# Kernel optimization log

Hardware: AMD Instinct MI355X
Metric: run time of the kernel (lower is better)

## Reference

```python
import jax, jax.numpy as jnp
import numpy as np

NUM_HEADS = 8
OUT_FEATS = 128
D_HEAD = OUT_FEATS // NUM_HEADS
N_NODES = 50000
N_EDGES = 600000
IN_FEATS = 128


def setup_inputs() -> dict:
    key = jax.random.key(0)
    ks = jax.random.split(key, 10)
    h = jax.random.normal(ks[0], (N_NODES, IN_FEATS), dtype=jnp.float32)
    src = jax.random.randint(ks[1], (N_EDGES,), 0, N_NODES)
    dst = jax.random.randint(ks[2], (N_EDGES,), 0, N_NODES)
    s = 1.0 / np.sqrt(IN_FEATS)
    W_Q = jax.random.normal(ks[3], (IN_FEATS, OUT_FEATS), dtype=jnp.float32) * s
    W_K = jax.random.normal(ks[4], (IN_FEATS, OUT_FEATS), dtype=jnp.float32) * s
    W_V = jax.random.normal(ks[5], (IN_FEATS, OUT_FEATS), dtype=jnp.float32) * s
    b_Q = jnp.zeros((OUT_FEATS,), dtype=jnp.float32)
    b_K = jnp.zeros((OUT_FEATS,), dtype=jnp.float32)
    b_V = jnp.zeros((OUT_FEATS,), dtype=jnp.float32)
    return {"h": h, "W_Q": W_Q, "b_Q": b_Q, "W_K": W_K, "b_K": b_K,
            "W_V": W_V, "b_V": b_V, "src": src, "dst": dst}


def _graph_conv(h, W, b, src, dst, norm_src, norm_dst):
    # DGL GraphConv, norm='both': D_dst^{-1/2} * A * D_src^{-1/2} * (h W) + b
    x = (h * norm_src[:, None]) @ W                              # [N, F]
    agg = jax.ops.segment_sum(x[src], dst, num_segments=h.shape[0])
    return agg * norm_dst[:, None] + b


def reference(h, W_Q, b_Q, W_K, b_K, W_V, b_V, src, dst):
    N = h.shape[0]
    ones = jnp.ones(src.shape[0], dtype=h.dtype)
    deg_out = jax.ops.segment_sum(ones, src, num_segments=N)   # out-degree (src side)
    deg_in = jax.ops.segment_sum(ones, dst, num_segments=N)    # in-degree (dst side)
    norm_src = jax.lax.rsqrt(jnp.clip(deg_out, 1.0))
    norm_dst = jax.lax.rsqrt(jnp.clip(deg_in, 1.0))

    Q = jax.nn.relu(_graph_conv(h, W_Q, b_Q, src, dst, norm_src, norm_dst))
    K = jax.nn.relu(_graph_conv(h, W_K, b_K, src, dst, norm_src, norm_dst))
    V = jax.nn.relu(_graph_conv(h, W_V, b_V, src, dst, norm_src, norm_dst))

    Qh = Q.reshape(N, NUM_HEADS, D_HEAD)
    Kh = K.reshape(N, NUM_HEADS, D_HEAD)
    Vh = V.reshape(N, NUM_HEADS, D_HEAD)

    # edge-wise scores: K at src dotted with Q at dst, per head
    score = jnp.sum(Kh[src] * Qh[dst], axis=-1, keepdims=True)   # [E, H, 1]
    score = jnp.exp(jnp.clip(score / np.sqrt(D_HEAD), -10.0, 10.0))

    wV = jax.ops.segment_sum(Vh[src] * score, dst, num_segments=N)  # [N, H, Dh]
    z = jax.ops.segment_sum(score, dst, num_segments=N)             # [N, H, 1]
    return wV / (z + 1e-6)
```

## Files before the change

kernel.cpp:

```cpp
#include <hip/hip_runtime.h>

#define INF  128
#define OUTF 128
#define NH   8
#define DHD  16
#define CAP  48

typedef __attribute__((ext_vector_type(8))) short bf16x8;
typedef __attribute__((ext_vector_type(4))) float f32x4;

__device__ __forceinline__ float bf16_to_f32(unsigned short u) {
    union { unsigned int i; float f; } v;
    v.i = ((unsigned int)u) << 16;
    return v.f;
}
__device__ __forceinline__ unsigned short f32_to_bf16(float f) {
    union { float f; unsigned int i; } v;
    v.f = f;
    unsigned int x = v.i;
    return (unsigned short)((x + 0x7fffu + ((x >> 16) & 1u)) >> 16);
}

__global__ void k_front(const int* __restrict__ src, const int* __restrict__ dst,
                        int* __restrict__ deg_out, int* __restrict__ cursor,
                        int* __restrict__ edge_src, int E, int SB, int HB,
                        const float* __restrict__ h, unsigned short* __restrict__ h_b, int N,
                        const float* __restrict__ Wq, const float* __restrict__ Wk,
                        const float* __restrict__ Wv, unsigned short* __restrict__ frag) {
    if (blockIdx.x < (unsigned)SB) {
        int t = blockIdx.x * 256 + threadIdx.x;
        int e0 = t * 4;
        if (e0 + 4 <= E) {
            int4 s4 = *reinterpret_cast<const int4*>(src + e0);
            int4 d4 = *reinterpret_cast<const int4*>(dst + e0);
            atomicAdd(&deg_out[s4.x], 1);
            atomicAdd(&deg_out[s4.y], 1);
            atomicAdd(&deg_out[s4.z], 1);
            atomicAdd(&deg_out[s4.w], 1);
            int p0 = atomicAdd(&cursor[d4.x], 1);
            int p1 = atomicAdd(&cursor[d4.y], 1);
            int p2 = atomicAdd(&cursor[d4.z], 1);
            int p3 = atomicAdd(&cursor[d4.w], 1);
            if (p0 < CAP) edge_src[d4.x * CAP + p0] = s4.x;
            if (p1 < CAP) edge_src[d4.y * CAP + p1] = s4.y;
            if (p2 < CAP) edge_src[d4.z * CAP + p2] = s4.z;
            if (p3 < CAP) edge_src[d4.w * CAP + p3] = s4.w;
        } else {
            for (int e = e0; e < E; ++e) {
                int s = src[e];
                int d = dst[e];
                atomicAdd(&deg_out[s], 1);
                int p = atomicAdd(&cursor[d], 1);
                if (p < CAP) edge_src[d * CAP + p] = s;
            }
        }
    } else if (blockIdx.x < (unsigned)(SB + HB)) {
        int t = (blockIdx.x - SB) * 256 + threadIdx.x;
        if (t < N * (INF / 8)) {
            const float4* p = reinterpret_cast<const float4*>(h + (size_t)t * 8);
            float4 v0 = p[0], v1 = p[1];
            uint4 o;
            o.x = (unsigned int)f32_to_bf16(v0.x) | ((unsigned int)f32_to_bf16(v0.y) << 16);
            o.y = (unsigned int)f32_to_bf16(v0.z) | ((unsigned int)f32_to_bf16(v0.w) << 16);
            o.z = (unsigned int)f32_to_bf16(v1.x) | ((unsigned int)f32_to_bf16(v1.y) << 16);
            o.w = (unsigned int)f32_to_bf16(v1.z) | ((unsigned int)f32_to_bf16(v1.w) << 16);
            *reinterpret_cast<uint4*>(h_b + (size_t)t * 8) = o;
        }
    } else {
        int t = (blockIdx.x - SB - HB) * 256 + threadIdx.x;
        if (t >= 3 * 8 * 4 * 2 * 64) return;
        int lane  = t & 63;
        int plane = (t >> 6) & 1;
        int ks    = (t >> 7) & 3;
        int nt    = (t >> 9) & 7;
        int mat   = t >> 12;
        const float* W = (mat == 0) ? Wq : ((mat == 1) ? Wk : Wv);
        int ln = lane & 15, quad = lane >> 4;
        int n = nt * 16 + ln;
        unsigned short vals[8];
        #pragma unroll
        for (int j = 0; j < 8; ++j) {
            int k = ks * 32 + quad * 8 + j;
            float a = W[k * OUTF + n];
            unsigned short hb = f32_to_bf16(a);
            vals[j] = plane ? f32_to_bf16(a - bf16_to_f32(hb)) : hb;
        }
        unsigned int* dp = reinterpret_cast<unsigned int*>(frag + (size_t)t * 8);
        #pragma unroll
        for (int j = 0; j < 4; ++j)
            dp[j] = (unsigned int)vals[2 * j] | ((unsigned int)vals[2 * j + 1] << 16);
    }
}

__global__ __launch_bounds__(256) void k_agg(const unsigned short* __restrict__ h_b,
                                             const int* __restrict__ deg_out,
                                             const int* __restrict__ cursor,
                                             const int* __restrict__ edge_src,
                                             float* __restrict__ agg, int N) {
    int wid  = (blockIdx.x * 256 + threadIdx.x) >> 6;
    int lane = threadIdx.x & 63;
    if (wid >= N) return;
    int slice = lane >> 4, li = lane & 15;
    int c8 = li * 8;
    float a0 = 0.f, a1 = 0.f, a2 = 0.f, a3 = 0.f;
    float a4 = 0.f, a5 = 0.f, a6 = 0.f, a7 = 0.f;
    int deg = cursor[wid]; if (deg > CAP) deg = CAP;
    const int* row = edge_src + wid * CAP;
    auto proc = [&](int e) {
        int s = row[e];
        int dg = deg_out[s]; if (dg < 1) dg = 1;
        float ns = rsqrtf((float)dg);
        uint4 p = *reinterpret_cast<const uint4*>(h_b + (size_t)s * INF + c8);
        a0 += ns * bf16_to_f32((unsigned short)(p.x & 0xffffu));
        a1 += ns * bf16_to_f32((unsigned short)(p.x >> 16));
        a2 += ns * bf16_to_f32((unsigned short)(p.y & 0xffffu));
        a3 += ns * bf16_to_f32((unsigned short)(p.y >> 16));
        a4 += ns * bf16_to_f32((unsigned short)(p.z & 0xffffu));
        a5 += ns * bf16_to_f32((unsigned short)(p.z >> 16));
        a6 += ns * bf16_to_f32((unsigned short)(p.w & 0xffffu));
        a7 += ns * bf16_to_f32((unsigned short)(p.w >> 16));
    };
    int e = slice;
    for (; e + 8 <= deg; e += 8) { proc(e); proc(e + 4); }
    for (; e < deg; e += 4) proc(e);
    a0 += __shfl_xor(a0, 16); a1 += __shfl_xor(a1, 16);
    a2 += __shfl_xor(a2, 16); a3 += __shfl_xor(a3, 16);
    a4 += __shfl_xor(a4, 16); a5 += __shfl_xor(a5, 16);
    a6 += __shfl_xor(a6, 16); a7 += __shfl_xor(a7, 16);
    a0 += __shfl_xor(a0, 32); a1 += __shfl_xor(a1, 32);
    a2 += __shfl_xor(a2, 32); a3 += __shfl_xor(a3, 32);
    a4 += __shfl_xor(a4, 32); a5 += __shfl_xor(a5, 32);
    a6 += __shfl_xor(a6, 32); a7 += __shfl_xor(a7, 32);
    if (slice == 0) {
        float* o = agg + (size_t)wid * INF + c8;
        *reinterpret_cast<float4*>(o)     = make_float4(a0, a1, a2, a3);
        *reinterpret_cast<float4*>(o + 4) = make_float4(a4, a5, a6, a7);
    }
}

__global__ __launch_bounds__(256) void k_gemm(const float* __restrict__ agg,
                                              const unsigned short* __restrict__ frag,
                                              const float* __restrict__ bq,
                                              const float* __restrict__ bk,
                                              const float* __restrict__ bv,
                                              const int* __restrict__ cursor,
                                              float* __restrict__ qbuf,
                                              unsigned short* __restrict__ kvbuf,
                                              int N) {
    int wave = threadIdx.x >> 6;
    int lane = threadIdx.x & 63;
    int ln   = lane & 15;
    int quad = lane >> 4;
    int mrow = blockIdx.x * 64 + wave * 16;

    bf16x8 ah[4], al[4];
    {
        int m = mrow + ln; if (m >= N) m = N - 1;
        const float* arow = agg + (size_t)m * INF;
        #pragma unroll
        for (int ks = 0; ks < 4; ++ks) {
            const float4* p = reinterpret_cast<const float4*>(arow + ks * 32 + quad * 8);
            float4 v0 = p[0], v1 = p[1];
            float vv[8] = {v0.x, v0.y, v0.z, v0.w, v1.x, v1.y, v1.z, v1.w};
            #pragma unroll
            for (int j = 0; j < 8; ++j) {
                unsigned short hb = f32_to_bf16(vv[j]);
                ah[ks][j] = (short)hb;
                al[ks][j] = (short)f32_to_bf16(vv[j] - bf16_to_f32(hb));
            }
        }
    }

    float nrm[4];
    #pragma unroll
    for (int r = 0; r < 4; ++r) {
        int m = mrow + quad * 4 + r;
        if (m < N) {
            int dg = cursor[m]; if (dg < 1) dg = 1;
            nrm[r] = rsqrtf((float)dg);
        } else nrm[r] = 0.f;
    }

    for (int mat = 0; mat < 3; ++mat) {
        const float* bb = (mat == 0) ? bq : ((mat == 1) ? bk : bv);
        #pragma unroll 2
        for (int nt = 0; nt < 8; ++nt) {
            int n0 = nt * 16;
            f32x4 acc = {0.f, 0.f, 0.f, 0.f};
            #pragma unroll
            for (int ks = 0; ks < 4; ++ks) {
                size_t base = ((size_t)(((mat * 8 + nt) * 4 + ks) * 2) * 64 + lane) * 8;
                bf16x8 bh = *reinterpret_cast<const bf16x8*>(frag + base);
                bf16x8 bl = *reinterpret_cast<const bf16x8*>(frag + base + 64 * 8);
                acc = __builtin_amdgcn_mfma_f32_16x16x32_bf16(ah[ks], bh, acc, 0, 0, 0);
                acc = __builtin_amdgcn_mfma_f32_16x16x32_bf16(al[ks], bh, acc, 0, 0, 0);
                acc = __builtin_amdgcn_mfma_f32_16x16x32_bf16(ah[ks], bl, acc, 0, 0, 0);
            }
            int col = n0 + ln;
            float bias = bb[col];
            #pragma unroll
            for (int r = 0; r < 4; ++r) {
                int m = mrow + quad * 4 + r;
                if (m < N) {
                    float v = acc[r] * nrm[r] + bias;
                    v = (v > 0.f) ? v : 0.f;
                    if (mat == 0) {
                        qbuf[(size_t)m * OUTF + col] = v;
                    } else {
                        int idx = ((col >> 2) << 3) + (col & 3) + ((mat == 2) ? 4 : 0);
                        kvbuf[(size_t)m * 2 * OUTF + idx] = f32_to_bf16(v);
                    }
                }
            }
        }
    }
}

__global__ __launch_bounds__(256) void k_attn(const float* __restrict__ qbuf,
                                              const unsigned short* __restrict__ kvbuf,
                                              const int* __restrict__ cursor,
                                              const int* __restrict__ edge_src,
                                              float* __restrict__ out, int N) {
    int wid  = (blockIdx.x * 256 + threadIdx.x) >> 6;
    int lane = threadIdx.x & 63;
    if (wid >= N) return;
    int half = lane >> 5, li = lane & 31;
    int c4 = li * 4;
    float4 q = *reinterpret_cast<const float4*>(qbuf + (size_t)wid * OUTF + c4);
    float a0 = 0.f, a1 = 0.f, a2 = 0.f, a3 = 0.f, z = 0.f;
    int deg = cursor[wid]; if (deg > CAP) deg = CAP;
    const int* row = edge_src + wid * CAP;
    auto proc = [&](int e) {
        int s = row[e];
        uint4 kp = *reinterpret_cast<const uint4*>(kvbuf + (size_t)s * 2 * OUTF + li * 8);
        float p = q.x * bf16_to_f32((unsigned short)(kp.x & 0xffffu))
                + q.y * bf16_to_f32((unsigned short)(kp.x >> 16))
                + q.z * bf16_to_f32((unsigned short)(kp.y & 0xffffu))
                + q.w * bf16_to_f32((unsigned short)(kp.y >> 16));
        p += __shfl_xor(p, 1);
        p += __shfl_xor(p, 2);
        float w = __expf(fminf(fmaxf(0.25f * p, -10.f), 10.f));
        z  += w;
        a0 += w * bf16_to_f32((unsigned short)(kp.z & 0xffffu));
        a1 += w * bf16_to_f32((unsigned short)(kp.z >> 16));
        a2 += w * bf16_to_f32((unsigned short)(kp.w & 0xffffu));
        a3 += w * bf16_to_f32((unsigned short)(kp.w >> 16));
    };
    int e = half;
    for (; e + 4 <= deg; e += 4) { proc(e); proc(e + 2); }
    for (; e < deg; e += 2) proc(e);
    a0 += __shfl_xor(a0, 32);
    a1 += __shfl_xor(a1, 32);
    a2 += __shfl_xor(a2, 32);
    a3 += __shfl_xor(a3, 32);
    z  += __shfl_xor(z, 32);
    if (half == 0) {
        float inv = 1.0f / (z + 1e-6f);
        *reinterpret_cast<float4*>(out + (size_t)wid * OUTF + c4) =
            make_float4(a0 * inv, a1 * inv, a2 * inv, a3 * inv);
    }
}

extern "C" void kernel_launch(void* const* d_in, const int* in_sizes, int n_in,
                              void* d_out, int out_size, void* d_ws, size_t ws_size,
                              hipStream_t stream) {
    const float* h  = (const float*)d_in[0];
    const float* Wq = (const float*)d_in[1];
    const float* bq = (const float*)d_in[2];
    const float* Wk = (const float*)d_in[3];
    const float* bk = (const float*)d_in[4];
    const float* Wv = (const float*)d_in[5];
    const float* bv = (const float*)d_in[6];
    const int* src = (const int*)d_in[7];
    const int* dst = (const int*)d_in[8];

    const int N = in_sizes[0] / INF;
    const int E = in_sizes[7];

    char* ws = (char*)d_ws;
    size_t off = 0;
    auto carve = [&](size_t bytes) -> void* {
        void* p = ws + off;
        off = (off + bytes + 255) & ~(size_t)255;
        return p;
    };
    int*   zeroed    = (int*)  carve((size_t)2 * N * sizeof(int));
    int*   deg_out   = zeroed;
    int*   cursor    = zeroed + N;
    int*   edge_src  = (int*)  carve((size_t)N * CAP * sizeof(int));
    unsigned short* h_b  = (unsigned short*)carve((size_t)N * INF * sizeof(unsigned short));
    float* agg       = (float*)carve((size_t)N * INF * sizeof(float));
    float* qbuf      = (float*)carve((size_t)N * OUTF * sizeof(float));
    unsigned short* kvbuf = (unsigned short*)carve((size_t)N * 2 * OUTF * sizeof(unsigned short));
    unsigned short* wfrag = (unsigned short*)carve((size_t)3 * 8 * 4 * 2 * 64 * 8 * sizeof(unsigned short));
    (void)ws_size;

    float* out = (float*)d_out;

    hipMemsetAsync(zeroed, 0, (size_t)2 * N * sizeof(int), stream);

    int SB = (E / 4 + 255) / 256 + 1;
    int HB = (N * (INF / 8) + 255) / 256;
    int WB = (3 * 8 * 4 * 2 * 64 + 255) / 256;
    k_front<<<SB + HB + WB, 256, 0, stream>>>(src, dst, deg_out, cursor, edge_src,
                                              E, SB, HB, h, h_b, N, Wq, Wk, Wv, wfrag);

    int gAgg = (N + 3) / 4;
    k_agg<<<gAgg, 256, 0, stream>>>(h_b, deg_out, cursor, edge_src, agg, N);

    int gT = (N + 63) / 64;
    k_gemm<<<gT, 256, 0, stream>>>(agg, wfrag, bq, bk, bv, cursor, qbuf, kvbuf, N);

    k_attn<<<gAgg, 256, 0, stream>>>(qbuf, kvbuf, cursor, edge_src, out, N);
}
```

Before: 273.7 us.

## Fuse all stages into one persistent cooperative kernel with grid syncs

Replaces the memset and four separate kernel launches with a single cooperative persistent kernel. Grid-stride loops cover each stage, and grid.sync() separates zeroing, edge bucketing and conversion, aggregation, the MFMA projection, and attention. The aim is to remove launch gaps and the memset. In exchange it adds grid-wide barrier overhead, a capped grid size that may lower latency hiding for the gather phases, and heavier register pressure because all phases live in one kernel.

```diff
diff --git a/kernel.cpp b/kernel.cpp
--- a/kernel.cpp
+++ b/kernel.cpp
@@ -1,4 +1,7 @@
 #include <hip/hip_runtime.h>
+#include <hip/hip_cooperative_groups.h>
+
+namespace cg = cooperative_groups;
 
 #define INF  128
 #define OUTF 128
@@ -21,15 +24,27 @@
     return (unsigned short)((x + 0x7fffu + ((x >> 16) & 1u)) >> 16);
 }
 
-__global__ void k_front(const int* __restrict__ src, const int* __restrict__ dst,
-                        int* __restrict__ deg_out, int* __restrict__ cursor,
-                        int* __restrict__ edge_src, int E, int SB, int HB,
-                        const float* __restrict__ h, unsigned short* __restrict__ h_b, int N,
-                        const float* __restrict__ Wq, const float* __restrict__ Wk,
-                        const float* __restrict__ Wv, unsigned short* __restrict__ frag) {
-    if (blockIdx.x < (unsigned)SB) {
-        int t = blockIdx.x * 256 + threadIdx.x;
-        int e0 = t * 4;
+__global__ __launch_bounds__(256, 4) void k_fused(
+        const int* __restrict__ src, const int* __restrict__ dst,
+        int* __restrict__ deg_out, int* __restrict__ cursor,
+        int* __restrict__ edge_src, int E,
+        const float* __restrict__ h, unsigned short* __restrict__ h_b, int N,
+        const float* __restrict__ Wq, const float* __restrict__ Wk,
+        const float* __restrict__ Wv, unsigned short* __restrict__ wfrag,
+        const float* __restrict__ bq, const float* __restrict__ bk,
+        const float* __restrict__ bv,
+        float* __restrict__ agg,
+        float* __restrict__ qbuf, unsigned short* __restrict__ kvbuf,
+        float* __restrict__ out) {
+    cg::grid_group grid = cg::this_grid();
+    const int T    = gridDim.x * 256;
+    const int gtid = blockIdx.x * 256 + threadIdx.x;
+    const int lane = threadIdx.x & 63;
+
+    for (int i = gtid; i < N; i += T) { deg_out[i] = 0; cursor[i] = 0; }
+    grid.sync();
+
+    for (int e0 = gtid * 4; e0 < E; e0 += T * 4) {
         if (e0 + 4 <= E) {
             int4 s4 = *reinterpret_cast<const int4*>(src + e0);
             int4 d4 = *reinterpret_cast<const int4*>(dst + e0);
@@ -54,210 +69,192 @@
                 if (p < CAP) edge_src[d * CAP + p] = s;
             }
         }
-    } else if (blockIdx.x < (unsigned)(SB + HB)) {
-        int t = (blockIdx.x - SB) * 256 + threadIdx.x;
-        if (t < N * (INF / 8)) {
-            const float4* p = reinterpret_cast<const float4*>(h + (size_t)t * 8);
-            float4 v0 = p[0], v1 = p[1];
-            uint4 o;
-            o.x = (unsigned int)f32_to_bf16(v0.x) | ((unsigned int)f32_to_bf16(v0.y) << 16);
-            o.y = (unsigned int)f32_to_bf16(v0.z) | ((unsigned int)f32_to_bf16(v0.w) << 16);
-            o.z = (unsigned int)f32_to_bf16(v1.x) | ((unsigned int)f32_to_bf16(v1.y) << 16);
-            o.w = (unsigned int)f32_to_bf16(v1.z) | ((unsigned int)f32_to_bf16(v1.w) << 16);
-            *reinterpret_cast<uint4*>(h_b + (size_t)t * 8) = o;
-        }
-    } else {
-        int t = (blockIdx.x - SB - HB) * 256 + threadIdx.x;
-        if (t >= 3 * 8 * 4 * 2 * 64) return;
-        int lane  = t & 63;
+    }
+    for (int t = gtid; t < N * (INF / 8); t += T) {
+        const float4* p = reinterpret_cast<const float4*>(h + (size_t)t * 8);
+        float4 v0 = p[0], v1 = p[1];
+        uint4 o;
+        o.x = (unsigned int)f32_to_bf16(v0.x) | ((unsigned int)f32_to_bf16(v0.y) << 16);
+        o.y = (unsigned int)f32_to_bf16(v0.z) | ((unsigned int)f32_to_bf16(v0.w) << 16);
+        o.z = (unsigned int)f32_to_bf16(v1.x) | ((unsigned int)f32_to_bf16(v1.y) << 16);
+        o.w = (unsigned int)f32_to_bf16(v1.z) | ((unsigned int)f32_to_bf16(v1.w) << 16);
+        *reinterpret_cast<uint4*>(h_b + (size_t)t * 8) = o;
+    }
+    for (int t = gtid; t < 3 * 8 * 4 * 2 * 64; t += T) {
+        int wl    = t & 63;
         int plane = (t >> 6) & 1;
         int ks    = (t >> 7) & 3;
         int nt    = (t >> 9) & 7;
         int mat   = t >> 12;
         const float* W = (mat == 0) ? Wq : ((mat == 1) ? Wk : Wv);
-        int ln = lane & 15, quad = lane >> 4;
-        int n = nt * 16 + ln;
+        int wln = wl & 15, wquad = wl >> 4;
+        int n = nt * 16 + wln;
         unsigned short vals[8];
         #pragma unroll
         for (int j = 0; j < 8; ++j) {
-            int k = ks * 32 + quad * 8 + j;
+            int k = ks * 32 + wquad * 8 + j;
             float a = W[k * OUTF + n];
             unsigned short hb = f32_to_bf16(a);
             vals[j] = plane ? f32_to_bf16(a - bf16_to_f32(hb)) : hb;
         }
-        unsigned int* dp = reinterpret_cast<unsigned int*>(frag + (size_t)t * 8);
+        unsigned int* dp = reinterpret_cast<unsigned int*>(wfrag + (size_t)t * 8);
         #pragma unroll
         for (int j = 0; j < 4; ++j)
             dp[j] = (unsigned int)vals[2 * j] | ((unsigned int)vals[2 * j + 1] << 16);
     }
-}
-
-__global__ __launch_bounds__(256) void k_agg(const unsigned short* __restrict__ h_b,
-                                             const int* __restrict__ deg_out,
-                                             const int* __restrict__ cursor,
-                                             const int* __restrict__ edge_src,
-                                             float* __restrict__ agg, int N) {
-    int wid  = (blockIdx.x * 256 + threadIdx.x) >> 6;
-    int lane = threadIdx.x & 63;
-    if (wid >= N) return;
-    int slice = lane >> 4, li = lane & 15;
-    int c8 = li * 8;
-    float a0 = 0.f, a1 = 0.f, a2 = 0.f, a3 = 0.f;
-    float a4 = 0.f, a5 = 0.f, a6 = 0.f, a7 = 0.f;
-    int deg = cursor[wid]; if (deg > CAP) deg = CAP;
-    const int* row = edge_src + wid * CAP;
-    auto proc = [&](int e) {
-        int s = row[e];
-        int dg = deg_out[s]; if (dg < 1) dg = 1;
-        float ns = rsqrtf((float)dg);
-        uint4 p = *reinterpret_cast<const uint4*>(h_b + (size_t)s * INF + c8);
-        a0 += ns * bf16_to_f32((unsigned short)(p.x & 0xffffu));
-        a1 += ns * bf16_to_f32((unsigned short)(p.x >> 16));
-        a2 += ns * bf16_to_f32((unsigned short)(p.y & 0xffffu));
-        a3 += ns * bf16_to_f32((unsigned short)(p.y >> 16));
-        a4 += ns * bf16_to_f32((unsigned short)(p.z & 0xffffu));
-        a5 += ns * bf16_to_f32((unsigned short)(p.z >> 16));
-        a6 += ns * bf16_to_f32((unsigned short)(p.w & 0xffffu));
-        a7 += ns * bf16_to_f32((unsigned short)(p.w >> 16));
-    };
-    int e = slice;
-    for (; e + 8 <= deg; e += 8) { proc(e); proc(e + 4); }
-    for (; e < deg; e += 4) proc(e);
-    a0 += __shfl_xor(a0, 16); a1 += __shfl_xor(a1, 16);
-    a2 += __shfl_xor(a2, 16); a3 += __shfl_xor(a3, 16);
-    a4 += __shfl_xor(a4, 16); a5 += __shfl_xor(a5, 16);
-    a6 += __shfl_xor(a6, 16); a7 += __shfl_xor(a7, 16);
-    a0 += __shfl_xor(a0, 32); a1 += __shfl_xor(a1, 32);
-    a2 += __shfl_xor(a2, 32); a3 += __shfl_xor(a3, 32);
-    a4 += __shfl_xor(a4, 32); a5 += __shfl_xor(a5, 32);
-    a6 += __shfl_xor(a6, 32); a7 += __shfl_xor(a7, 32);
-    if (slice == 0) {
-        float* o = agg + (size_t)wid * INF + c8;
-        *reinterpret_cast<float4*>(o)     = make_float4(a0, a1, a2, a3);
-        *reinterpret_cast<float4*>(o + 4) = make_float4(a4, a5, a6, a7);
-    }
-}
-
-__global__ __launch_bounds__(256) void k_gemm(const float* __restrict__ agg,
-                                              const unsigned short* __restrict__ frag,
-                                              const float* __restrict__ bq,
-                                              const float* __restrict__ bk,
-                                              const float* __restrict__ bv,
-                                              const int* __restrict__ cursor,
-                                              float* __restrict__ qbuf,
-                                              unsigned short* __restrict__ kvbuf,
-                                              int N) {
-    int wave = threadIdx.x >> 6;
-    int lane = threadIdx.x & 63;
-    int ln   = lane & 15;
-    int quad = lane >> 4;
-    int mrow = blockIdx.x * 64 + wave * 16;
-
-    bf16x8 ah[4], al[4];
+    grid.sync();
+
     {
-        int m = mrow + ln; if (m >= N) m = N - 1;
-        const float* arow = agg + (size_t)m * INF;
-        #pragma unroll
-        for (int ks = 0; ks < 4; ++ks) {
-            const float4* p = reinterpret_cast<const float4*>(arow + ks * 32 + quad * 8);
-            float4 v0 = p[0], v1 = p[1];
-            float vv[8] = {v0.x, v0.y, v0.z, v0.w, v1.x, v1.y, v1.z, v1.w};
-            #pragma unroll
-            for (int j = 0; j < 8; ++j) {
-                unsigned short hb = f32_to_bf16(vv[j]);
-                ah[ks][j] = (short)hb;
-                al[ks][j] = (short)f32_to_bf16(vv[j] - bf16_to_f32(hb));
-            }
-        }
-    }
-
-    float nrm[4];
-    #pragma unroll
-    for (int r = 0; r < 4; ++r) {
-        int m = mrow + quad * 4 + r;
-        if (m < N) {
-            int dg = cursor[m]; if (dg < 1) dg = 1;
-            nrm[r] = rsqrtf((float)dg);
-        } else nrm[r] = 0.f;
-    }
-
-    for (int mat = 0; mat < 3; ++mat) {
-        const float* bb = (mat == 0) ? bq : ((mat == 1) ? bk : bv);
-        #pragma unroll 2
-        for (int nt = 0; nt < 8; ++nt) {
-            int n0 = nt * 16;
-            f32x4 acc = {0.f, 0.f, 0.f, 0.f};
-            #pragma unroll
-            for (int ks = 0; ks < 4; ++ks) {
-                size_t base = ((size_t)(((mat * 8 + nt) * 4 + ks) * 2) * 64 + lane) * 8;
-                bf16x8 bh = *reinterpret_cast<const bf16x8*>(frag + base);
-                bf16x8 bl = *reinterpret_cast<const bf16x8*>(frag + base + 64 * 8);
-                acc = __builtin_amdgcn_mfma_f32_16x16x32_bf16(ah[ks], bh, acc, 0, 0, 0);
-                acc = __builtin_amdgcn_mfma_f32_16x16x32_bf16(al[ks], bh, acc, 0, 0, 0);
-                acc = __builtin_amdgcn_mfma_f32_16x16x32_bf16(ah[ks], bl, acc, 0, 0, 0);
-            }
-            int col = n0 + ln;
-            float bias = bb[col];
+        int wv = gtid >> 6, nw = T >> 6;
+        int slice = lane >> 4, li = lane & 15;
+        int c8 = li * 8;
+        for (int wid = wv; wid < N; wid += nw) {
+            float a0 = 0.f, a1 = 0.f, a2 = 0.f, a3 = 0.f;
+            float a4 = 0.f, a5 = 0.f, a6 = 0.f, a7 = 0.f;
+            int deg = cursor[wid]; if (deg > CAP) deg = CAP;
+            const int* row = edge_src + wid * CAP;
+            auto proc = [&](int e) {
+                int s = row[e];
+                int dg = deg_out[s]; if (dg < 1) dg = 1;
+                float ns = rsqrtf((float)dg);
+                uint4 p = *reinterpret_cast<const uint4*>(h_b + (size_t)s * INF + c8);
+                a0 += ns * bf16_to_f32((unsigned short)(p.x & 0xffffu));
+                a1 += ns * bf16_to_f32((unsigned short)(p.x >> 16));
+                a2 += ns * bf16_to_f32((unsigned short)(p.y & 0xffffu));
+                a3 += ns * bf16_to_f32((unsigned short)(p.y >> 16));
+                a4 += ns * bf16_to_f32((unsigned short)(p.z & 0xffffu));
+                a5 += ns * bf16_to_f32((unsigned short)(p.z >> 16));
+                a6 += ns * bf16_to_f32((unsigned short)(p.w & 0xffffu));
+                a7 += ns * bf16_to_f32((unsigned short)(p.w >> 16));
+            };
+            int e = slice;
+            for (; e + 8 <= deg; e += 8) { proc(e); proc(e + 4); }
+            for (; e < deg; e += 4) proc(e);
+            a0 += __shfl_xor(a0, 16); a1 += __shfl_xor(a1, 16);
+            a2 += __shfl_xor(a2, 16); a3 += __shfl_xor(a3, 16);
+            a4 += __shfl_xor(a4, 16); a5 += __shfl_xor(a5, 16);
+            a6 += __shfl_xor(a6, 16); a7 += __shfl_xor(a7, 16);
+            a0 += __shfl_xor(a0, 32); a1 += __shfl_xor(a1, 32);
+            a2 += __shfl_xor(a2, 32); a3 += __shfl_xor(a3, 32);
+            a4 += __shfl_xor(a4, 32); a5 += __shfl_xor(a5, 32);
+            a6 += __shfl_xor(a6, 32); a7 += __shfl_xor(a7, 32);
+            if (slice == 0) {
+                float* o = agg + (size_t)wid * INF + c8;
+                *reinterpret_cast<float4*>(o)     = make_float4(a0, a1, a2, a3);
+                *reinterpret_cast<float4*>(o + 4) = make_float4(a4, a5, a6, a7);
+            }
+        }
+    }
+    grid.sync();
+
+    {
+        int wave = threadIdx.x >> 6;
+        int ln   = lane & 15;
+        int quad = lane >> 4;
+        for (int tile = blockIdx.x; tile * 64 < N; tile += gridDim.x) {
+            int mrow = tile * 64 + wave * 16;
+            bf16x8 ah[4], al[4];
+            {
+                int m = mrow + ln; if (m >= N) m = N - 1;
+                const float* arow = agg + (size_t)m * INF;
+                #pragma unroll
+                for (int ks = 0; ks < 4; ++ks) {
+                    const float4* p = reinterpret_cast<const float4*>(arow + ks * 32 + quad * 8);
+                    float4 v0 = p[0], v1 = p[1];
+                    float vv[8] = {v0.x, v0.y, v0.z, v0.w, v1.x, v1.y, v1.z, v1.w};
+                    #pragma unroll
+                    for (int j = 0; j < 8; ++j) {
+                        unsigned short hb = f32_to_bf16(vv[j]);
+                        ah[ks][j] = (short)hb;
+                        al[ks][j] = (short)f32_to_bf16(vv[j] - bf16_to_f32(hb));
+                    }
+                }
+            }
+            float nrm[4];
             #pragma unroll
             for (int r = 0; r < 4; ++r) {
                 int m = mrow + quad * 4 + r;
                 if (m < N) {
-                    float v = acc[r] * nrm[r] + bias;
-                    v = (v > 0.f) ? v : 0.f;
-                    if (mat == 0) {
-                        qbuf[(size_t)m * OUTF + col] = v;
-                    } else {
-                        int idx = ((col >> 2) << 3) + (col & 3) + ((mat == 2) ? 4 : 0);
-                        kvbuf[(size_t)m * 2 * OUTF + idx] = f32_to_bf16(v);
+                    int dg = cursor[m]; if (dg < 1) dg = 1;
+                    nrm[r] = rsqrtf((float)dg);
+                } else nrm[r] = 0.f;
+            }
+            for (int mat = 0; mat < 3; ++mat) {
+                const float* bb = (mat == 0) ? bq : ((mat == 1) ? bk : bv);
+                #pragma unroll 2
+                for (int nt = 0; nt < 8; ++nt) {
+                    int n0 = nt * 16;
+                    f32x4 acc = {0.f, 0.f, 0.f, 0.f};
+                    #pragma unroll
+                    for (int ks = 0; ks < 4; ++ks) {
+                        size_t base = ((size_t)(((mat * 8 + nt) * 4 + ks) * 2) * 64 + lane) * 8;
+                        bf16x8 bh = *reinterpret_cast<const bf16x8*>(wfrag + base);
+                        bf16x8 bl = *reinterpret_cast<const bf16x8*>(wfrag + base + 64 * 8);
+                        acc = __builtin_amdgcn_mfma_f32_16x16x32_bf16(ah[ks], bh, acc, 0, 0, 0);
+                        acc = __builtin_amdgcn_mfma_f32_16x16x32_bf16(al[ks], bh, acc, 0, 0, 0);
+                        acc = __builtin_amdgcn_mfma_f32_16x16x32_bf16(ah[ks], bl, acc, 0, 0, 0);
+                    }
+                    int col = n0 + ln;
+                    float bias = bb[col];
+                    #pragma unroll
+                    for (int r = 0; r < 4; ++r) {
+                        int m = mrow + quad * 4 + r;
+                        if (m < N) {
+                            float v = acc[r] * nrm[r] + bias;
+                            v = (v > 0.f) ? v : 0.f;
+                            if (mat == 0) {
+                                qbuf[(size_t)m * OUTF + col] = v;
+                            } else {
+                                int idx = ((col >> 2) << 3) + (col & 3) + ((mat == 2) ? 4 : 0);
+                                kvbuf[(size_t)m * 2 * OUTF + idx] = f32_to_bf16(v);
+                            }
+                        }
                     }
                 }
             }
         }
     }
-}
-
-__global__ __launch_bounds__(256) void k_attn(const float* __restrict__ qbuf,
-                                              const unsigned short* __restrict__ kvbuf,
-                                              const int* __restrict__ cursor,
-                                              const int* __restrict__ edge_src,
-                                              float* __restrict__ out, int N) {
-    int wid  = (blockIdx.x * 256 + threadIdx.x) >> 6;
-    int lane = threadIdx.x & 63;
-    if (wid >= N) return;
-    int half = lane >> 5, li = lane & 31;
-    int c4 = li * 4;
-    float4 q = *reinterpret_cast<const float4*>(qbuf + (size_t)wid * OUTF + c4);
-    float a0 = 0.f, a1 = 0.f, a2 = 0.f, a3 = 0.f, z = 0.f;
-    int deg = cursor[wid]; if (deg > CAP) deg = CAP;
-    const int* row = edge_src + wid * CAP;
-    auto proc = [&](int e) {
-        int s = row[e];
-        uint4 kp = *reinterpret_cast<const uint4*>(kvbuf + (size_t)s * 2 * OUTF + li * 8);
-        float p = q.x * bf16_to_f32((unsigned short)(kp.x & 0xffffu))
-                + q.y * bf16_to_f32((unsigned short)(kp.x >> 16))
-                + q.z * bf16_to_f32((unsigned short)(kp.y & 0xffffu))
-                + q.w * bf16_to_f32((unsigned short)(kp.y >> 16));
-        p += __shfl_xor(p, 1);
-        p += __shfl_xor(p, 2);
-        float w = __expf(fminf(fmaxf(0.25f * p, -10.f), 10.f));
-        z  += w;
-        a0 += w * bf16_to_f32((unsigned short)(kp.z & 0xffffu));
-        a1 += w * bf16_to_f32((unsigned short)(kp.z >> 16));
-        a2 += w * bf16_to_f32((unsigned short)(kp.w & 0xffffu));
-        a3 += w * bf16_to_f32((unsigned short)(kp.w >> 16));
-    };
-    int e = half;
-    for (; e + 4 <= deg; e += 4) { proc(e); proc(e + 2); }
-    for (; e < deg; e += 2) proc(e);
-    a0 += __shfl_xor(a0, 32);
-    a1 += __shfl_xor(a1, 32);
-    a2 += __shfl_xor(a2, 32);
-    a3 += __shfl_xor(a3, 32);
-    z  += __shfl_xor(z, 32);
-    if (half == 0) {
-        float inv = 1.0f / (z + 1e-6f);
-        *reinterpret_cast<float4*>(out + (size_t)wid * OUTF + c4) =
-            make_float4(a0 * inv, a1 * inv, a2 * inv, a3 * inv);
+    grid.sync();
+
+    {
+        int wv = gtid >> 6, nw = T >> 6;
+        int half = lane >> 5, li = lane & 31;
+        int c4 = li * 4;
+        for (int wid = wv; wid < N; wid += nw) {
+            float4 q = *reinterpret_cast<const float4*>(qbuf + (size_t)wid * OUTF + c4);
+            float a0 = 0.f, a1 = 0.f, a2 = 0.f, a3 = 0.f, z = 0.f;
+            int deg = cursor[wid]; if (deg > CAP) deg = CAP;
+            const int* row = edge_src + wid * CAP;
+            auto proc = [&](int e) {
+                int s = row[e];
+                uint4 kp = *reinterpret_cast<const uint4*>(kvbuf + (size_t)s * 2 * OUTF + li * 8);
+                float p = q.x * bf16_to_f32((unsigned short)(kp.x & 0xffffu))
+                        + q.y * bf16_to_f32((unsigned short)(kp.x >> 16))
+                        + q.z * bf16_to_f32((unsigned short)(kp.y & 0xffffu))
+                        + q.w * bf16_to_f32((unsigned short)(kp.y >> 16));
+                p += __shfl_xor(p, 1);
+                p += __shfl_xor(p, 2);
+                float w = __expf(fminf(fmaxf(0.25f * p, -10.f), 10.f));
+                z  += w;
+                a0 += w * bf16_to_f32((unsigned short)(kp.z & 0xffffu));
+                a1 += w * bf16_to_f32((unsigned short)(kp.z >> 16));
+                a2 += w * bf16_to_f32((unsigned short)(kp.w & 0xffffu));
+                a3 += w * bf16_to_f32((unsigned short)(kp.w >> 16));
+            };
+            int e = half;
+            for (; e + 4 <= deg; e += 4) { proc(e); proc(e + 2); }
+            for (; e < deg; e += 2) proc(e);
+            a0 += __shfl_xor(a0, 32);
+            a1 += __shfl_xor(a1, 32);
+            a2 += __shfl_xor(a2, 32);
+            a3 += __shfl_xor(a3, 32);
+            z  += __shfl_xor(z, 32);
+            if (half == 0) {
+                float inv = 1.0f / (z + 1e-6f);
+                *reinterpret_cast<float4*>(out + (size_t)wid * OUTF + c4) =
+                    make_float4(a0 * inv, a1 * inv, a2 * inv, a3 * inv);
+            }
+        }
     }
 }
 
@@ -274,8 +271,8 @@
     const int* src = (const int*)d_in[7];
     const int* dst = (const int*)d_in[8];
 
-    const int N = in_sizes[0] / INF;
-    const int E = in_sizes[7];
+    int N = in_sizes[0] / INF;
+    int E = in_sizes[7];
 
     char* ws = (char*)d_ws;
     size_t off = 0;
@@ -284,9 +281,8 @@
         off = (off + bytes + 255) & ~(size_t)255;
         return p;
     };
-    int*   zeroed    = (int*)  carve((size_t)2 * N * sizeof(int));
-    int*   deg_out   = zeroed;
-    int*   cursor    = zeroed + N;
+    int*   deg_out   = (int*)  carve((size_t)N * sizeof(int));
+    int*   cursor    = (int*)  carve((size_t)N * sizeof(int));
     int*   edge_src  = (int*)  carve((size_t)N * CAP * sizeof(int));
     unsigned short* h_b  = (unsigned short*)carve((size_t)N * INF * sizeof(unsigned short));
     float* agg       = (float*)carve((size_t)N * INF * sizeof(float));
@@ -297,19 +293,19 @@
 
     float* out = (float*)d_out;
 
-    hipMemsetAsync(zeroed, 0, (size_t)2 * N * sizeof(int), stream);
-
-    int SB = (E / 4 + 255) / 256 + 1;
-    int HB = (N * (INF / 8) + 255) / 256;
-    int WB = (3 * 8 * 4 * 2 * 64 + 255) / 256;
-    k_front<<<SB + HB + WB, 256, 0, stream>>>(src, dst, deg_out, cursor, edge_src,
-                                              E, SB, HB, h, h_b, N, Wq, Wk, Wv, wfrag);
-
-    int gAgg = (N + 3) / 4;
-    k_agg<<<gAgg, 256, 0, stream>>>(h_b, deg_out, cursor, edge_src, agg, N);
-
-    int gT = (N + 63) / 64;
-    k_gemm<<<gT, 256, 0, stream>>>(agg, wfrag, bq, bk, bv, cursor, qbuf, kvbuf, N);
-
-    k_attn<<<gAgg, 256, 0, stream>>>(qbuf, kvbuf, cursor, edge_src, out, N);
+    int occ = 0;
+    hipOccupancyMaxActiveBlocksPerMultiprocessor(&occ, k_fused, 256, 0);
+    if (occ < 1) occ = 1;
+    long long grid_ll = (long long)occ * 256;
+    if (grid_ll > 2048) grid_ll = 2048;
+    int grid = (int)grid_ll;
+
+    void* args[] = {
+        (void*)&src, (void*)&dst, (void*)&deg_out, (void*)&cursor,
+        (void*)&edge_src, (void*)&E, (void*)&h, (void*)&h_b, (void*)&N,
+        (void*)&Wq, (void*)&Wk, (void*)&Wv, (void*)&wfrag,
+        (void*)&bq, (void*)&bk, (void*)&bv,
+        (void*)&agg, (void*)&qbuf, (void*)&kvbuf, (void*)&out
+    };
+    hipLaunchCooperativeKernel((void*)k_fused, dim3(grid), dim3(256), args, 0, stream);
 }
```

Result: slower. 603.6 us (+120.6%).
